# Kernel tuning notes

Measured on AMD Instinct MI355X. Metric: run time of the kernel, lower is better.

## Reference

```python
import jax, jax.numpy as jnp
import numpy as np

NUM_EMBEDDINGS = 8192
EMBEDDING_DIM = 256
COMMITMENT_COST = 0.25


def setup_inputs() -> dict:
    key = jax.random.key(0)
    k1, k2 = jax.random.split(key)
    z_e = jax.random.normal(k1, (16, 2048, EMBEDDING_DIM), dtype=jnp.float32)
    # nn.Embedding init: uniform(-1/K, 1/K)
    codebook = jax.random.uniform(
        k2, (NUM_EMBEDDINGS, EMBEDDING_DIM), dtype=jnp.float32,
        minval=-1.0 / NUM_EMBEDDINGS, maxval=1.0 / NUM_EMBEDDINGS)
    return {"z_e": z_e, "codebook": codebook}


def _nearest_indices(z_flat, codebook):
    # squared euclidean distances; argmin is identical to argmin of cdist
    # z_flat: [T, D], codebook: [K, D] -> dist2: [T, K]
    x2 = jnp.sum(z_flat * z_flat, axis=-1, keepdims=True)          # [T, 1]
    w2 = jnp.sum(codebook * codebook, axis=-1)                      # [K]
    xw = jnp.einsum('td,kd->tk', z_flat, codebook)                  # [T, K]
    dist2 = x2 - 2.0 * xw + w2
    return jnp.argmin(dist2, axis=1)                                # [T]


def reference(z_e, codebook):
    original_shape = z_e.shape
    z_e_flat = z_e.reshape(-1, EMBEDDING_DIM)
    indices = _nearest_indices(z_e_flat, codebook)
    z_q = codebook[indices].reshape(original_shape)
    # straight-through estimator
    z_q_ste = z_e + jax.lax.stop_gradient(z_q - z_e)
    commitment_loss = jnp.mean((z_e - jax.lax.stop_gradient(z_q_ste)) ** 2)
    codebook_loss = jnp.mean((z_q_ste - jax.lax.stop_gradient(z_e)) ** 2)
    loss = codebook_loss + COMMITMENT_COST * commitment_loss
    # codebook usage: fraction of unique indices (jit-friendly via scatter)
    used = jnp.zeros((NUM_EMBEDDINGS,), dtype=jnp.float32).at[indices].set(1.0)
    usage = jnp.sum(used) / NUM_EMBEDDINGS
    return (z_q_ste, loss, usage)
```

## Files before the change

kernel.cpp:

```cpp
#include <hip/hip_runtime.h>
#include <float.h>

#define T_TOTAL 32768
#define KC      8192
#define DIM     256

#define LOSS_IDX  ((size_t)T_TOTAL * DIM)
#define USAGE_IDX (LOSS_IDX + 1)

typedef short s16x8 __attribute__((ext_vector_type(8)));
typedef float f32x4 __attribute__((ext_vector_type(4)));

#define WS_W2    0
#define WS_FLAGS 32768
#define WS_ZBF   65536
#define WS_CBF   (65536 + 16777216)

__device__ __forceinline__ unsigned short f2bf(float f) {
    unsigned int u = __float_as_uint(f);
    u += 0x7FFFu + ((u >> 16) & 1u);
    return (unsigned short)(u >> 16);
}

__global__ __launch_bounds__(256) void vq_prep(const float* __restrict__ z_e,
                                               const float* __restrict__ cb,
                                               unsigned short* __restrict__ zb,
                                               unsigned short* __restrict__ cbb,
                                               float* __restrict__ w2,
                                               int* __restrict__ flags,
                                               float* __restrict__ out) {
    const int blk = blockIdx.x, tid = threadIdx.x;
    if (blk < 4096) {
        size_t i = ((size_t)blk * 256 + tid) * 8;
        float4 a = *(const float4*)(z_e + i);
        float4 b = *(const float4*)(z_e + i + 4);
        uint4 o;
        o.x = (unsigned)f2bf(a.x) | ((unsigned)f2bf(a.y) << 16);
        o.y = (unsigned)f2bf(a.z) | ((unsigned)f2bf(a.w) << 16);
        o.z = (unsigned)f2bf(b.x) | ((unsigned)f2bf(b.y) << 16);
        o.w = (unsigned)f2bf(b.z) | ((unsigned)f2bf(b.w) << 16);
        *(uint4*)(zb + i) = o;
        if (blk < 32) flags[blk * 256 + tid] = 0;
        if (blk == 0 && tid == 0) { out[LOSS_IDX] = 0.0f; out[USAGE_IDX] = 0.0f; }
    } else {
        size_t base = (size_t)(blk - 4096) * 2048;
        size_t i = base + (size_t)tid * 8;
        float4 a = *(const float4*)(cb + i);
        float4 b = *(const float4*)(cb + i + 4);
        uint4 o;
        o.x = (unsigned)f2bf(a.x) | ((unsigned)f2bf(a.y) << 16);
        o.y = (unsigned)f2bf(a.z) | ((unsigned)f2bf(a.w) << 16);
        o.z = (unsigned)f2bf(b.x) | ((unsigned)f2bf(b.y) << 16);
        o.w = (unsigned)f2bf(b.z) | ((unsigned)f2bf(b.w) << 16);
        *(uint4*)(cbb + i) = o;
        float s = a.x * a.x + a.y * a.y + a.z * a.z + a.w * a.w
                + b.x * b.x + b.y * b.y + b.z * b.z + b.w * b.w;
        #pragma unroll
        for (int m = 1; m <= 16; m <<= 1) s += __shfl_xor(s, m);
        if ((tid & 31) == 0) w2[(blk - 4096) * 8 + (tid >> 5)] = s;
    }
}

__global__ __launch_bounds__(512, 2) void vq_main(const unsigned short* __restrict__ zb,
                                                  const unsigned short* __restrict__ cbb,
                                                  const float* __restrict__ w2g,
                                                  const float* __restrict__ z_e,
                                                  const float* __restrict__ cb,
                                                  float* __restrict__ out,
                                                  int* __restrict__ flags) {
    __shared__ unsigned short ca[128 * 128];
    __shared__ unsigned long long smin[128];
    __shared__ float wls[8];

    const int tid  = threadIdx.x;
    const int lane = tid & 63;
    const int w    = tid >> 6;
    const int wr   = w >> 1;
    const int wc   = w & 1;
    const int quad = lane >> 4;
    const int l15  = lane & 15;
    const int t0   = blockIdx.x * 128;

    if (tid < 128) smin[tid] = ~0ULL;

    s16x8 af[2][8];
    #pragma unroll
    for (int i = 0; i < 2; ++i)
        #pragma unroll
        for (int ks = 0; ks < 8; ++ks)
            af[i][ks] = *(const s16x8*)(zb + (size_t)(t0 + wr * 32 + i * 16 + l15) * DIM + ks * 32 + quad * 8);

    float best[2][4];
    int   bidx[2][4];
    #pragma unroll
    for (int i = 0; i < 2; ++i)
        #pragma unroll
        for (int r = 0; r < 4; ++r) { best[i][r] = FLT_MAX; bidx[i][r] = 0x7FFFFFFF; }

    for (int c0 = 0; c0 < KC; c0 += 128) {
        f32x4 acc[2][4];
        #pragma unroll
        for (int i = 0; i < 2; ++i)
            #pragma unroll
            for (int j = 0; j < 4; ++j) acc[i][j] = (f32x4){0.f, 0.f, 0.f, 0.f};

        #pragma unroll
        for (int kw = 0; kw < 2; ++kw) {
            __syncthreads();
            #pragma unroll
            for (int r = 0; r < 4; ++r) {
                int rowbase = r * 32 + w * 4;
                int row = rowbase + (lane >> 4);
                int src_c = (lane & 15) ^ (row & 15);
                __builtin_amdgcn_global_load_lds(
                    (const __attribute__((address_space(1))) void*)(cbb + (size_t)(c0 + row) * DIM + kw * 128 + src_c * 8),
                    (__attribute__((address_space(3))) void*)(ca + rowbase * 128),
                    16, 0, 0);
            }
            __syncthreads();

            #pragma unroll
            for (int kk = 0; kk < 4; ++kk) {
                s16x8 bfr[4];
                #pragma unroll
                for (int j = 0; j < 4; ++j) {
                    int row = wc * 64 + j * 16 + l15;
                    int slot = (kk * 4 + quad) ^ l15;
                    bfr[j] = *(const s16x8*)(ca + row * 128 + slot * 8);
                }
                #pragma unroll
                for (int i = 0; i < 2; ++i)
                    #pragma unroll
                    for (int j = 0; j < 4; ++j)
                        acc[i][j] = __builtin_amdgcn_mfma_f32_16x16x32_bf16(af[i][kw * 4 + kk], bfr[j], acc[i][j], 0, 0, 0);
            }
        }

        #pragma unroll
        for (int j = 0; j < 4; ++j) {
            int col = c0 + wc * 64 + j * 16 + l15;
            float w2v = w2g[col];
            #pragma unroll
            for (int i = 0; i < 2; ++i)
                #pragma unroll
                for (int r = 0; r < 4; ++r) {
                    float s = fmaf(-2.0f, acc[i][j][r], w2v);
                    if (s < best[i][r]) { best[i][r] = s; bidx[i][r] = col; }
                }
        }
    }

    #pragma unroll
    for (int i = 0; i < 2; ++i)
        #pragma unroll
        for (int r = 0; r < 4; ++r) {
            float b = best[i][r]; int ix = bidx[i][r];
            #pragma unroll
            for (int m = 1; m < 16; m <<= 1) {
                float ob = __shfl_xor(b, m);
                int   oi = __shfl_xor(ix, m);
                if (ob < b || (ob == b && oi < ix)) { b = ob; ix = oi; }
            }
            if (l15 == 0) {
                unsigned int fb = __float_as_uint(b);
                fb = (fb & 0x80000000u) ? ~fb : (fb | 0x80000000u);
                unsigned long long key = ((unsigned long long)fb << 32) | (unsigned int)ix;
                atomicMin(&smin[wr * 32 + i * 16 + quad * 4 + r], key);
            }
        }
    __syncthreads();

    float lsum = 0.0f;
    for (int t = w * 16; t < w * 16 + 16; ++t) {
        int tok = t0 + t;
        int k = (int)(unsigned int)(smin[t] & 0xFFFFFFFFull);
        if (lane == 0) flags[k] = 1;
        float4 c = *(const float4*)(cb + (size_t)k * DIM + lane * 4);
        float4 z = *(const float4*)(z_e + (size_t)tok * DIM + lane * 4);
        float dx = z.x - c.x, dy = z.y - c.y, dz = z.z - c.z, dw = z.w - c.w;
        lsum += dx * dx + dy * dy + dz * dz + dw * dw;
        *(float4*)(out + (size_t)tok * DIM + lane * 4) = c;
    }
    #pragma unroll
    for (int m = 32; m >= 1; m >>= 1) lsum += __shfl_xor(lsum, m);
    if (lane == 0) wls[w] = lsum;
    __syncthreads();
    if (tid == 0) {
        float bsum = 0.0f;
        #pragma unroll
        for (int q = 0; q < 8; ++q) bsum += wls[q];
        atomicAdd(out + LOSS_IDX, bsum * (1.25f / (float)LOSS_IDX));
    }
}

__global__ __launch_bounds__(256) void vq_usage(const int* __restrict__ flags,
                                                float* __restrict__ out) {
    __shared__ int ws[4];
    int tid = threadIdx.x;
    int s = 0;
    for (int i = tid; i < KC; i += 256) s += flags[i];
    #pragma unroll
    for (int m = 32; m >= 1; m >>= 1) s += __shfl_xor(s, m);
    if ((tid & 63) == 0) ws[tid >> 6] = s;
    __syncthreads();
    if (tid == 0) out[USAGE_IDX] = (float)(ws[0] + ws[1] + ws[2] + ws[3]) / (float)KC;
}

extern "C" void kernel_launch(void* const* d_in, const int* in_sizes, int n_in,
                              void* d_out, int out_size, void* d_ws, size_t ws_size,
                              hipStream_t stream) {
    (void)in_sizes; (void)n_in; (void)out_size; (void)ws_size;
    const float* z_e = (const float*)d_in[0];
    const float* cb  = (const float*)d_in[1];
    float* out = (float*)d_out;

    char* ws = (char*)d_ws;
    float* w2    = (float*)(ws + WS_W2);
    int*   flags = (int*)(ws + WS_FLAGS);
    unsigned short* zb  = (unsigned short*)(ws + WS_ZBF);
    unsigned short* cbb = (unsigned short*)(ws + WS_CBF);

    vq_prep<<<4096 + 1024, 256, 0, stream>>>(z_e, cb, zb, cbb, w2, flags, out);
    vq_main<<<T_TOTAL / 128, 512, 0, stream>>>(zb, cbb, w2, z_e, cb, out, flags);
    vq_usage<<<1, 256, 0, stream>>>(flags, out);
}
```

Baseline: 280.8 us.

## Double-buffer codebook LDS tiles, fuse z bf16 conversion, retile waves 2x4

The z_e bf16 conversion pass and its workspace buffer are removed; each block now converts its own z rows to bf16 in registers when loading its A fragments. The codebook LDS tile becomes double-buffered, so the next half-tile's async global-to-LDS load is issued before computing on the current one, removing one barrier per step. The wave layout changes from 4x2 to 2x4, so each wave holds 64 token rows and 32 codes. The aim is to cut the prep kernel's memory traffic and overlap loads with MFMA work. In exchange, the A fragments double to 128 VGPRs under a 512-thread, 2-blocks-per-CU launch bound, which risks register spills, and LDS use doubles to 64 KB per block.

```diff
diff --git a/kernel.cpp b/kernel.cpp
--- a/kernel.cpp
+++ b/kernel.cpp
@@ -13,8 +13,7 @@
 
 #define WS_W2    0
 #define WS_FLAGS 32768
-#define WS_ZBF   65536
-#define WS_CBF   (65536 + 16777216)
+#define WS_CBF   65536
 
 __device__ __forceinline__ unsigned short f2bf(float f) {
     unsigned int u = __float_as_uint(f);
@@ -22,126 +21,131 @@
     return (unsigned short)(u >> 16);
 }
 
-__global__ __launch_bounds__(256) void vq_prep(const float* __restrict__ z_e,
-                                               const float* __restrict__ cb,
-                                               unsigned short* __restrict__ zb,
+__global__ __launch_bounds__(256) void vq_prep(const float* __restrict__ cb,
                                                unsigned short* __restrict__ cbb,
                                                float* __restrict__ w2,
                                                int* __restrict__ flags,
                                                float* __restrict__ out) {
     const int blk = blockIdx.x, tid = threadIdx.x;
-    if (blk < 4096) {
-        size_t i = ((size_t)blk * 256 + tid) * 8;
-        float4 a = *(const float4*)(z_e + i);
-        float4 b = *(const float4*)(z_e + i + 4);
-        uint4 o;
-        o.x = (unsigned)f2bf(a.x) | ((unsigned)f2bf(a.y) << 16);
-        o.y = (unsigned)f2bf(a.z) | ((unsigned)f2bf(a.w) << 16);
-        o.z = (unsigned)f2bf(b.x) | ((unsigned)f2bf(b.y) << 16);
-        o.w = (unsigned)f2bf(b.z) | ((unsigned)f2bf(b.w) << 16);
-        *(uint4*)(zb + i) = o;
-        if (blk < 32) flags[blk * 256 + tid] = 0;
-        if (blk == 0 && tid == 0) { out[LOSS_IDX] = 0.0f; out[USAGE_IDX] = 0.0f; }
-    } else {
-        size_t base = (size_t)(blk - 4096) * 2048;
-        size_t i = base + (size_t)tid * 8;
-        float4 a = *(const float4*)(cb + i);
-        float4 b = *(const float4*)(cb + i + 4);
-        uint4 o;
-        o.x = (unsigned)f2bf(a.x) | ((unsigned)f2bf(a.y) << 16);
-        o.y = (unsigned)f2bf(a.z) | ((unsigned)f2bf(a.w) << 16);
-        o.z = (unsigned)f2bf(b.x) | ((unsigned)f2bf(b.y) << 16);
-        o.w = (unsigned)f2bf(b.z) | ((unsigned)f2bf(b.w) << 16);
-        *(uint4*)(cbb + i) = o;
-        float s = a.x * a.x + a.y * a.y + a.z * a.z + a.w * a.w
-                + b.x * b.x + b.y * b.y + b.z * b.z + b.w * b.w;
-        #pragma unroll
-        for (int m = 1; m <= 16; m <<= 1) s += __shfl_xor(s, m);
-        if ((tid & 31) == 0) w2[(blk - 4096) * 8 + (tid >> 5)] = s;
-    }
-}
-
-__global__ __launch_bounds__(512, 2) void vq_main(const unsigned short* __restrict__ zb,
-                                                  const unsigned short* __restrict__ cbb,
+    size_t i = (size_t)blk * 2048 + (size_t)tid * 8;
+    float4 a = *(const float4*)(cb + i);
+    float4 b = *(const float4*)(cb + i + 4);
+    uint4 o;
+    o.x = (unsigned)f2bf(a.x) | ((unsigned)f2bf(a.y) << 16);
+    o.y = (unsigned)f2bf(a.z) | ((unsigned)f2bf(a.w) << 16);
+    o.z = (unsigned)f2bf(b.x) | ((unsigned)f2bf(b.y) << 16);
+    o.w = (unsigned)f2bf(b.z) | ((unsigned)f2bf(b.w) << 16);
+    *(uint4*)(cbb + i) = o;
+    float s = a.x * a.x + a.y * a.y + a.z * a.z + a.w * a.w
+            + b.x * b.x + b.y * b.y + b.z * b.z + b.w * b.w;
+    #pragma unroll
+    for (int m = 1; m <= 16; m <<= 1) s += __shfl_xor(s, m);
+    if ((tid & 31) == 0) w2[blk * 8 + (tid >> 5)] = s;
+    if (blk < 32) flags[blk * 256 + tid] = 0;
+    if (blk == 0 && tid == 0) { out[LOSS_IDX] = 0.0f; out[USAGE_IDX] = 0.0f; }
+}
+
+__global__ __launch_bounds__(512, 2) void vq_main(const unsigned short* __restrict__ cbb,
                                                   const float* __restrict__ w2g,
                                                   const float* __restrict__ z_e,
                                                   const float* __restrict__ cb,
                                                   float* __restrict__ out,
                                                   int* __restrict__ flags) {
-    __shared__ unsigned short ca[128 * 128];
+    __shared__ unsigned short ca[2][128 * 128];
     __shared__ unsigned long long smin[128];
     __shared__ float wls[8];
 
     const int tid  = threadIdx.x;
     const int lane = tid & 63;
     const int w    = tid >> 6;
-    const int wr   = w >> 1;
-    const int wc   = w & 1;
+    const int wr   = w >> 2;
+    const int wc   = w & 3;
     const int quad = lane >> 4;
     const int l15  = lane & 15;
     const int t0   = blockIdx.x * 128;
 
     if (tid < 128) smin[tid] = ~0ULL;
 
-    s16x8 af[2][8];
-    #pragma unroll
-    for (int i = 0; i < 2; ++i)
-        #pragma unroll
-        for (int ks = 0; ks < 8; ++ks)
-            af[i][ks] = *(const s16x8*)(zb + (size_t)(t0 + wr * 32 + i * 16 + l15) * DIM + ks * 32 + quad * 8);
-
-    float best[2][4];
-    int   bidx[2][4];
-    #pragma unroll
-    for (int i = 0; i < 2; ++i)
+    const int srow_off = lane >> 4;
+    #define STAGE(CHUNK, KW, P)                                                         \
+        {                                                                               \
+            _Pragma("unroll")                                                           \
+            for (int r = 0; r < 4; ++r) {                                               \
+                int rowbase = r * 32 + w * 4;                                           \
+                int row = rowbase + srow_off;                                           \
+                int src_c = l15 ^ (row & 15);                                           \
+                __builtin_amdgcn_global_load_lds(                                       \
+                    (const __attribute__((address_space(1))) void*)                     \
+                        (cbb + (size_t)((CHUNK) * 128 + row) * DIM + (KW) * 128 + src_c * 8), \
+                    (__attribute__((address_space(3))) void*)(ca[P] + rowbase * 128),   \
+                    16, 0, 0);                                                          \
+            }                                                                           \
+        }
+
+    s16x8 af[4][8];
+    #pragma unroll
+    for (int i = 0; i < 4; ++i) {
+        #pragma unroll
+        for (int ks = 0; ks < 8; ++ks) {
+            const float* p = z_e + (size_t)(t0 + wr * 64 + i * 16 + l15) * DIM + ks * 32 + quad * 8;
+            float4 a = *(const float4*)p;
+            float4 b = *(const float4*)(p + 4);
+            s16x8 v;
+            v[0] = (short)f2bf(a.x); v[1] = (short)f2bf(a.y);
+            v[2] = (short)f2bf(a.z); v[3] = (short)f2bf(a.w);
+            v[4] = (short)f2bf(b.x); v[5] = (short)f2bf(b.y);
+            v[6] = (short)f2bf(b.z); v[7] = (short)f2bf(b.w);
+            af[i][ks] = v;
+        }
+    }
+
+    float best[4][4];
+    int   bidx[4][4];
+    #pragma unroll
+    for (int i = 0; i < 4; ++i)
         #pragma unroll
         for (int r = 0; r < 4; ++r) { best[i][r] = FLT_MAX; bidx[i][r] = 0x7FFFFFFF; }
 
-    for (int c0 = 0; c0 < KC; c0 += 128) {
-        f32x4 acc[2][4];
-        #pragma unroll
-        for (int i = 0; i < 2; ++i)
-            #pragma unroll
-            for (int j = 0; j < 4; ++j) acc[i][j] = (f32x4){0.f, 0.f, 0.f, 0.f};
+    STAGE(0, 0, 0);
+
+    for (int c = 0; c < 64; ++c) {
+        f32x4 acc[4][2];
+        #pragma unroll
+        for (int i = 0; i < 4; ++i)
+            #pragma unroll
+            for (int j = 0; j < 2; ++j) acc[i][j] = (f32x4){0.f, 0.f, 0.f, 0.f};
 
         #pragma unroll
         for (int kw = 0; kw < 2; ++kw) {
             __syncthreads();
-            #pragma unroll
-            for (int r = 0; r < 4; ++r) {
-                int rowbase = r * 32 + w * 4;
-                int row = rowbase + (lane >> 4);
-                int src_c = (lane & 15) ^ (row & 15);
-                __builtin_amdgcn_global_load_lds(
-                    (const __attribute__((address_space(1))) void*)(cbb + (size_t)(c0 + row) * DIM + kw * 128 + src_c * 8),
-                    (__attribute__((address_space(3))) void*)(ca + rowbase * 128),
-                    16, 0, 0);
-            }
-            __syncthreads();
-
+            if (kw == 0) {
+                STAGE(c, 1, 1);
+            } else if (c < 63) {
+                STAGE(c + 1, 0, 0);
+            }
             #pragma unroll
             for (int kk = 0; kk < 4; ++kk) {
-                s16x8 bfr[4];
+                s16x8 bfr[2];
                 #pragma unroll
-                for (int j = 0; j < 4; ++j) {
-                    int row = wc * 64 + j * 16 + l15;
+                for (int j = 0; j < 2; ++j) {
+                    int row = wc * 32 + j * 16 + l15;
                     int slot = (kk * 4 + quad) ^ l15;
-                    bfr[j] = *(const s16x8*)(ca + row * 128 + slot * 8);
+                    bfr[j] = *(const s16x8*)(ca[kw] + row * 128 + slot * 8);
                 }
                 #pragma unroll
-                for (int i = 0; i < 2; ++i)
+                for (int i = 0; i < 4; ++i)
                     #pragma unroll
-                    for (int j = 0; j < 4; ++j)
+                    for (int j = 0; j < 2; ++j)
                         acc[i][j] = __builtin_amdgcn_mfma_f32_16x16x32_bf16(af[i][kw * 4 + kk], bfr[j], acc[i][j], 0, 0, 0);
             }
         }
 
         #pragma unroll
-        for (int j = 0; j < 4; ++j) {
-            int col = c0 + wc * 64 + j * 16 + l15;
+        for (int j = 0; j < 2; ++j) {
+            int col = c * 128 + wc * 32 + j * 16 + l15;
             float w2v = w2g[col];
             #pragma unroll
-            for (int i = 0; i < 2; ++i)
+            for (int i = 0; i < 4; ++i)
                 #pragma unroll
                 for (int r = 0; r < 4; ++r) {
                     float s = fmaf(-2.0f, acc[i][j][r], w2v);
@@ -151,7 +155,7 @@
     }
 
     #pragma unroll
-    for (int i = 0; i < 2; ++i)
+    for (int i = 0; i < 4; ++i)
         #pragma unroll
         for (int r = 0; r < 4; ++r) {
             float b = best[i][r]; int ix = bidx[i][r];
@@ -165,7 +169,7 @@
                 unsigned int fb = __float_as_uint(b);
                 fb = (fb & 0x80000000u) ? ~fb : (fb | 0x80000000u);
                 unsigned long long key = ((unsigned long long)fb << 32) | (unsigned int)ix;
-                atomicMin(&smin[wr * 32 + i * 16 + quad * 4 + r], key);
+                atomicMin(&smin[wr * 64 + i * 16 + quad * 4 + r], key);
             }
         }
     __syncthreads();
@@ -175,11 +179,11 @@
         int tok = t0 + t;
         int k = (int)(unsigned int)(smin[t] & 0xFFFFFFFFull);
         if (lane == 0) flags[k] = 1;
-        float4 c = *(const float4*)(cb + (size_t)k * DIM + lane * 4);
-        float4 z = *(const float4*)(z_e + (size_t)tok * DIM + lane * 4);
-        float dx = z.x - c.x, dy = z.y - c.y, dz = z.z - c.z, dw = z.w - c.w;
+        float4 cv = *(const float4*)(cb + (size_t)k * DIM + lane * 4);
+        float4 zv = *(const float4*)(z_e + (size_t)tok * DIM + lane * 4);
+        float dx = zv.x - cv.x, dy = zv.y - cv.y, dz = zv.z - cv.z, dw = zv.w - cv.w;
         lsum += dx * dx + dy * dy + dz * dz + dw * dw;
-        *(float4*)(out + (size_t)tok * DIM + lane * 4) = c;
+        *(float4*)(out + (size_t)tok * DIM + lane * 4) = cv;
     }
     #pragma unroll
     for (int m = 32; m >= 1; m >>= 1) lsum += __shfl_xor(lsum, m);
@@ -217,10 +221,9 @@
     char* ws = (char*)d_ws;
     float* w2    = (float*)(ws + WS_W2);
     int*   flags = (int*)(ws + WS_FLAGS);
-    unsigned short* zb  = (unsigned short*)(ws + WS_ZBF);
     unsigned short* cbb = (unsigned short*)(ws + WS_CBF);
 
-    vq_prep<<<4096 + 1024, 256, 0, stream>>>(z_e, cb, zb, cbb, w2, flags, out);
-    vq_main<<<T_TOTAL / 128, 512, 0, stream>>>(zb, cbb, w2, z_e, cb, out, flags);
+    vq_prep<<<KC / 8, 256, 0, stream>>>(cb, cbb, w2, flags, out);
+    vq_main<<<T_TOTAL / 128, 512, 0, stream>>>(cbb, w2, z_e, cb, out, flags);
     vq_usage<<<1, 256, 0, stream>>>(flags, out);
 }
```

New measurement: 265.5 us. 1.06x faster.
